# Kernel tuning notes

Hardware: AMD Instinct MI355X
Metric: run time of the kernel (lower is better)

## Reference

```python
import jax, jax.numpy as jnp
import numpy as np
from jax import lax

H = 1024      # hidden_size
M = 256       # memory_size
NH = 4        # num_heads
HD = M // NH  # head_dim = 64
EPS = 1e-5


def _ln(x, g, b):
    mu = jnp.mean(x, axis=-1, keepdims=True)
    var = jnp.mean(jnp.square(x - mu), axis=-1, keepdims=True)
    return (x - mu) * lax.rsqrt(var + EPS) * g + b


def setup_inputs() -> dict:
    key = jax.random.key(0)
    ks = jax.random.split(key, 12)
    B, S, NM = 8, 2048, 4096
    s = 0.02
    return {
        "query_hidden": jax.random.normal(ks[0], (B, S, H), jnp.float32),
        "mem_keys": jax.random.normal(ks[1], (NM, M), jnp.float32),
        "selection_scores": jax.random.uniform(ks[2], (NM,), jnp.float32),
        "qp_w": jax.random.normal(ks[3], (M, H), jnp.float32) * s,
        "qp_b": jnp.zeros((M,), jnp.float32),
        "in_proj_w": jax.random.normal(ks[4], (3 * M, M), jnp.float32) * s,
        "in_proj_b": jnp.zeros((3 * M,), jnp.float32),
        "out_w": jax.random.normal(ks[5], (M, M), jnp.float32) * s,
        "out_b": jnp.zeros((M,), jnp.float32),
        "gate_w": jax.random.normal(ks[6], (H, H + M), jnp.float32) * s,
        "gate_b": jnp.zeros((H,), jnp.float32),
        "int_w1": jax.random.normal(ks[7], (2 * H, H + M), jnp.float32) * s,
        "int_b1": jnp.zeros((2 * H,), jnp.float32),
        "int_ln_g": jnp.ones((2 * H,), jnp.float32),
        "int_ln_b": jnp.zeros((2 * H,), jnp.float32),
        "int_w2": jax.random.normal(ks[8], (H, 2 * H), jnp.float32) * s,
        "int_b2": jnp.zeros((H,), jnp.float32),
        "ln1_g": jnp.ones((M,), jnp.float32),
        "ln1_b": jnp.zeros((M,), jnp.float32),
        "ln2_g": jnp.ones((H,), jnp.float32),
        "ln2_b": jnp.zeros((H,), jnp.float32),
        "top_k": 512,
    }


def reference(query_hidden, mem_keys, selection_scores, qp_w, qp_b,
              in_proj_w, in_proj_b, out_w, out_b, gate_w, gate_b,
              int_w1, int_b1, int_ln_g, int_ln_b, int_w2, int_b2,
              ln1_g, ln1_b, ln2_g, ln2_b, top_k):
    B, S, _ = query_hidden.shape
    # query projection into memory space: [B,S,M]
    q_emb = query_hidden @ qp_w.T + qp_b
    # top-k memory selection by scores (static k)
    _, idx = lax.top_k(selection_scores, top_k)
    mem = mem_keys[idx]                      # [K, M]
    mem = _ln(mem, ln1_g, ln1_b)
    # MultiheadAttention (batch_first, eval mode). Per-position loop in the
    # original is equivalent to one batched attention (no mask).
    wq, wk, wv = jnp.split(in_proj_w, 3, axis=0)
    bq, bk, bv = jnp.split(in_proj_b, 3, axis=0)
    q = (q_emb @ wq.T + bq).reshape(B, S, NH, HD)
    k = (mem @ wk.T + bk).reshape(-1, NH, HD)   # [K,NH,HD]
    v = (mem @ wv.T + bv).reshape(-1, NH, HD)
    scores = jnp.einsum('bshd,khd->bhsk', q, k) / np.sqrt(HD).astype(jnp.float32)
    attn = jax.nn.softmax(scores, axis=-1)
    ctx = jnp.einsum('bhsk,khd->bshd', attn, v).reshape(B, S, M)
    attn_out = ctx @ out_w.T + out_b            # [B,S,M]
    # gated integration
    cat = jnp.concatenate([query_hidden, attn_out], axis=-1)  # [B,S,H+M]
    gate = jax.nn.sigmoid(cat @ gate_w.T + gate_b)
    h = _ln(cat @ int_w1.T + int_b1, int_ln_g, int_ln_b)
    h = jax.nn.gelu(h, approximate=False)
    integrated = h @ int_w2.T + int_b2
    out = _ln(query_hidden + gate * integrated, ln2_g, ln2_b)
    return out
```

## Files before the change

kernel.cpp:

```cpp
#include <hip/hip_runtime.h>
#include <math.h>


typedef __bf16 bf16x8 __attribute__((ext_vector_type(8)));
typedef __bf16 bf16x4 __attribute__((ext_vector_type(4)));
typedef float  floatx4 __attribute__((ext_vector_type(4)));

#define NMEM   4096
#define KSEL   512

__device__ __forceinline__ void gl_lds16(const __bf16* g, __bf16* l) {
  __builtin_amdgcn_global_load_lds(
      (const __attribute__((address_space(1))) void*)g,
      (__attribute__((address_space(3))) void*)l, 16, 0, 0);
}

__global__ void cvt_kernel(const float* __restrict__ s0, const float* __restrict__ s1,
                           const float* __restrict__ s2, const float* __restrict__ s3,
                           const float* __restrict__ s4,
                           __bf16* __restrict__ d0, __bf16* __restrict__ d1,
                           __bf16* __restrict__ d2, __bf16* __restrict__ d3,
                           __bf16* __restrict__ d4) {
  long q = (long)blockIdx.x * 256 + threadIdx.x;
  const long n0 = 16777216 / 4, n1 = 65536 / 4, n2 = 1310720 / 4,
             n3 = 2621440 / 4, n4 = 2097152 / 4;
  const float* s; __bf16* d; long off;
  if (q < n0) { s = s0; d = d0; off = q; }
  else if ((q -= n0) < n1) { s = s1; d = d1; off = q; }
  else if ((q -= n1) < n2) { s = s2; d = d2; off = q; }
  else if ((q -= n2) < n3) { s = s3; d = d3; off = q; }
  else if ((q -= n3) < n4) { s = s4; d = d4; off = q; }
  else return;
  float4 v = ((const float4*)s)[off];
  bf16x4 o;
  o[0] = (__bf16)v.x; o[1] = (__bf16)v.y; o[2] = (__bf16)v.z; o[3] = (__bf16)v.w;
  ((bf16x4*)d)[off] = o;
}

__device__ __forceinline__ unsigned mapbits(float x) {
  unsigned b = __float_as_uint(x);
  return (b & 0x80000000u) ? ~b : (b | 0x80000000u);
}

__global__ void topk_kernel(const float* __restrict__ scores, int* __restrict__ idx_out) {
  const int n = NMEM, k = KSEL;
  __shared__ int hist[256];
  __shared__ int s_need;
  __shared__ unsigned s_prefix;
  __shared__ int s_cnt_gt, s_ntie;
  __shared__ int tie[1024];
  int tid = threadIdx.x;
  if (tid == 0) { s_need = k; s_prefix = 0; s_cnt_gt = 0; s_ntie = 0; }
  __syncthreads();
  for (int pass = 0; pass < 4; ++pass) {
    if (tid < 256) hist[tid] = 0;
    __syncthreads();
    int shift = 24 - 8 * pass;
    unsigned pref = s_prefix;
    for (int i = tid; i < n; i += 256) {
      unsigned u = mapbits(scores[i]);
      bool in = (pass == 0) || ((u >> (shift + 8)) == pref);
      if (in) atomicAdd(&hist[(u >> shift) & 255], 1);
    }
    __syncthreads();
    if (tid == 0) {
      int need = s_need, above = 0, b = 255;
      for (;; --b) {
        int c = hist[b];
        if (above + c >= need) { s_need = need - above; break; }
        above += c;
      }
      s_prefix = (s_prefix << 8) | (unsigned)b;
    }
    __syncthreads();
  }
  unsigned T = s_prefix;
  int need = s_need;
  for (int i = tid; i < n; i += 256) {
    unsigned u = mapbits(scores[i]);
    if (u > T) { int p = atomicAdd(&s_cnt_gt, 1); idx_out[p] = i; }
    else if (u == T) { int t = atomicAdd(&s_ntie, 1); if (t < 1024) tie[t] = i; }
  }
  __syncthreads();
  int base = s_cnt_gt;
  int nt = s_ntie < 1024 ? s_ntie : 1024;
  for (int j = tid; j < nt; j += 256) {
    int my = tie[j], rank = 0;
    for (int l = 0; l < nt; ++l) rank += (tie[l] < my) ? 1 : 0;
    if (rank < need) idx_out[base + rank] = my;
  }
}

__global__ void wc_build(const float* __restrict__ qp_w, const float* __restrict__ qp_b,
                         const float* __restrict__ in_w, const float* __restrict__ in_b,
                         __bf16* __restrict__ Wc, float* __restrict__ bcq) {
  int i = blockIdx.x, t = threadIdx.x;
  const float* wq = in_w + (long)i * 256;
  float a0 = 0, a1 = 0, a2 = 0, a3 = 0;
  for (int s = 0; s < 256; ++s) {
    float wv = wq[s];
    const float* qr = qp_w + (long)s * 1024 + t;
    a0 += wv * qr[0];   a1 += wv * qr[256];
    a2 += wv * qr[512]; a3 += wv * qr[768];
  }
  __bf16* wr = Wc + (long)i * 1024 + t;
  wr[0]   = (__bf16)(0.125f * a0); wr[256] = (__bf16)(0.125f * a1);
  wr[512] = (__bf16)(0.125f * a2); wr[768] = (__bf16)(0.125f * a3);
  if (t == 0) {
    float s = in_b[i];
    for (int j = 0; j < 256; ++j) s += wq[j] * qp_b[j];
    bcq[i] = 0.125f * s;
  }
}

__global__ void kv_build(const int* __restrict__ idx, const float* __restrict__ mem_keys,
                         const float* __restrict__ in_w, const float* __restrict__ in_b,
                         const float* __restrict__ ln1g, const float* __restrict__ ln1b,
                         __bf16* __restrict__ Kmat, __bf16* __restrict__ Vt) {
  int r = blockIdx.x, t = threadIdx.x;
  int lane = t & 63, wave = t >> 6;
  __shared__ float wred[8];
  __shared__ float m[256];
  int row = idx[r];
  float x = mem_keys[(long)row * 256 + t];
  float s = x;
  #pragma unroll
  for (int o = 32; o > 0; o >>= 1) s += __shfl_xor(s, o);
  if (lane == 0) wred[wave] = s;
  __syncthreads();
  float mu = (wred[0] + wred[1] + wred[2] + wred[3]) / 256.0f;
  float e = x - mu;
  s = e * e;
  #pragma unroll
  for (int o = 32; o > 0; o >>= 1) s += __shfl_xor(s, o);
  if (lane == 0) wred[4 + wave] = s;
  __syncthreads();
  float rstd = rsqrtf((wred[4] + wred[5] + wred[6] + wred[7]) / 256.0f + 1e-5f);
  m[t] = e * rstd * ln1g[t] + ln1b[t];
  __syncthreads();
  float ka = 0.f, va = 0.f;
  const float* wk = in_w + (long)(256 + t) * 256;
  const float* wv = in_w + (long)(512 + t) * 256;
  #pragma unroll 4
  for (int i = 0; i < 256; i += 4) {
    float4 wkv = *(const float4*)(wk + i);
    float4 wvv = *(const float4*)(wv + i);
    ka += m[i] * wkv.x + m[i + 1] * wkv.y + m[i + 2] * wkv.z + m[i + 3] * wkv.w;
    va += m[i] * wvv.x + m[i + 1] * wvv.y + m[i + 2] * wvv.z + m[i + 3] * wvv.w;
  }
  ka += in_b[256 + t]; va += in_b[512 + t];
  Kmat[(long)r * 256 + t] = (__bf16)ka;
  Vt[(long)(t >> 6) * (64 * 512) + (long)(t & 63) * 512 + r] = (__bf16)va;
}

template <int BM, int BN, int EPI>
__launch_bounds__(256, 4)
__global__ void gemm_kernel(const __bf16* __restrict__ X1, int ldx1, int K1,
                            const __bf16* __restrict__ X2, int ldx2,
                            const __bf16* __restrict__ W, int ldw,
                            const float* __restrict__ bias,
                            __bf16* __restrict__ C, int ldc, int Ktot,
                            long sXz, long sWz, long sCz) {
  constexpr int BK = 64;
  __shared__ __bf16 As[BM * BK];
  __shared__ __bf16 Bs[BN * BK];
  const int tid = threadIdx.x;
  const int lane = tid & 63, wave = tid >> 6;
  const int wm = wave >> 1, wn = wave & 1;
  constexpr int FM = (BM / 2) / 16, FN = (BN / 2) / 16;
  floatx4 acc[FM][FN];
  #pragma unroll
  for (int i = 0; i < FM; ++i)
    #pragma unroll
    for (int j = 0; j < FN; ++j)
      #pragma unroll
      for (int r = 0; r < 4; ++r) acc[i][j][r] = 0.0f;

  const long z = blockIdx.z;
  const __bf16* x1 = X1 + z * sXz;
  const __bf16* w  = W + z * sWz;
  __bf16* c = C + z * sCz;
  const long row0 = (long)blockIdx.x * BM;
  const int col0 = blockIdx.y * BN;
  const int nKt = Ktot / BK;
  const int srow = lane >> 3;
  const int scol = ((lane & 7) ^ srow) * 8;

  for (int kt = 0; kt < nKt; ++kt) {
    const int k0 = kt * BK;
    const __bf16* xb; long xld; int kx;
    if (k0 < K1) { xb = x1; xld = ldx1; kx = k0; }
    else         { xb = X2; xld = ldx2; kx = k0 - K1; }
    #pragma unroll
    for (int i = 0; i < BM / 32; ++i) {
      int chunk = wave * (BM / 32) + i;
      const __bf16* g = xb + (row0 + chunk * 8 + srow) * xld + kx + scol;
      gl_lds16(g, As + chunk * 512);
    }
    #pragma unroll
    for (int i = 0; i < BN / 32; ++i) {
      int chunk = wave * (BN / 32) + i;
      const __bf16* g = w + (long)(col0 + chunk * 8 + srow) * ldw + k0 + scol;
      gl_lds16(g, Bs + chunk * 512);
    }
    __syncthreads();
    #pragma unroll
    for (int kk = 0; kk < 2; ++kk) {
      bf16x8 a[FM], b[FN];
      const int ccq = kk * 4 + (lane >> 4);
      #pragma unroll
      for (int fm = 0; fm < FM; ++fm) {
        const int r = wm * (BM / 2) + fm * 16 + (lane & 15);
        a[fm] = *(const bf16x8*)(As + r * BK + ((ccq ^ (r & 7)) << 3));
      }
      #pragma unroll
      for (int fn = 0; fn < FN; ++fn) {
        const int r = wn * (BN / 2) + fn * 16 + (lane & 15);
        b[fn] = *(const bf16x8*)(Bs + r * BK + ((ccq ^ (r & 7)) << 3));
      }
      #pragma unroll
      for (int fm = 0; fm < FM; ++fm)
        #pragma unroll
        for (int fn = 0; fn < FN; ++fn)
          acc[fm][fn] = __builtin_amdgcn_mfma_f32_16x16x32_bf16(a[fm], b[fn], acc[fm][fn], 0, 0, 0);
    }
    __syncthreads();
  }
  #pragma unroll
  for (int fn = 0; fn < FN; ++fn) {
    const int col = col0 + wn * (BN / 2) + fn * 16 + (lane & 15);
    float bv = (EPI == 1) ? 0.0f : bias[col];
    #pragma unroll
    for (int fm = 0; fm < FM; ++fm) {
      #pragma unroll
      for (int r = 0; r < 4; ++r) {
        long row = row0 + wm * (BM / 2) + fm * 16 + (lane >> 4) * 4 + r;
        float v = acc[fm][fn][r] + bv;
        if (EPI == 2) v = 1.0f / (1.0f + __expf(-v));
        c[row * (long)ldc + col] = (__bf16)v;
      }
    }
  }
}

__global__ void softmax_kernel(__bf16* __restrict__ S) {
  long row = (long)blockIdx.x * 4 + (threadIdx.x >> 6);
  int lane = threadIdx.x & 63;
  __bf16* p = S + row * 512 + lane * 8;
  bf16x8 v = *(const bf16x8*)p;
  float f[8], mx = -1e30f;
  #pragma unroll
  for (int j = 0; j < 8; ++j) { f[j] = (float)v[j]; mx = fmaxf(mx, f[j]); }
  #pragma unroll
  for (int o = 32; o > 0; o >>= 1) mx = fmaxf(mx, __shfl_xor(mx, o));
  float s = 0.f;
  #pragma unroll
  for (int j = 0; j < 8; ++j) { f[j] = __expf(f[j] - mx); s += f[j]; }
  #pragma unroll
  for (int o = 32; o > 0; o >>= 1) s += __shfl_xor(s, o);
  float inv = 1.0f / s;
  bf16x8 o8;
  #pragma unroll
  for (int j = 0; j < 8; ++j) o8[j] = (__bf16)(f[j] * inv);
  *(bf16x8*)p = o8;
}

__global__ void ln_gelu_kernel(__bf16* __restrict__ T1, const float* __restrict__ g,
                               const float* __restrict__ b) {
  long row = blockIdx.x; int t = threadIdx.x;
  int lane = t & 63, wave = t >> 6;
  __shared__ float wred[8];
  __bf16* p = T1 + row * 2048 + t * 8;
  bf16x8 v = *(const bf16x8*)p;
  float f[8], s = 0.f;
  #pragma unroll
  for (int j = 0; j < 8; ++j) { f[j] = (float)v[j]; s += f[j]; }
  #pragma unroll
  for (int o = 32; o > 0; o >>= 1) s += __shfl_xor(s, o);
  if (lane == 0) wred[wave] = s;
  __syncthreads();
  float mu = (wred[0] + wred[1] + wred[2] + wred[3]) / 2048.0f;
  s = 0.f;
  #pragma unroll
  for (int j = 0; j < 8; ++j) { f[j] -= mu; s += f[j] * f[j]; }
  #pragma unroll
  for (int o = 32; o > 0; o >>= 1) s += __shfl_xor(s, o);
  if (lane == 0) wred[4 + wave] = s;
  __syncthreads();
  float rstd = rsqrtf((wred[4] + wred[5] + wred[6] + wred[7]) / 2048.0f + 1e-5f);
  float4 g0 = *(const float4*)(g + t * 8), g1 = *(const float4*)(g + t * 8 + 4);
  float4 b0 = *(const float4*)(b + t * 8), b1 = *(const float4*)(b + t * 8 + 4);
  float gg[8] = { g0.x, g0.y, g0.z, g0.w, g1.x, g1.y, g1.z, g1.w };
  float bb[8] = { b0.x, b0.y, b0.z, b0.w, b1.x, b1.y, b1.z, b1.w };
  bf16x8 o8;
  #pragma unroll
  for (int j = 0; j < 8; ++j) {
    float y = f[j] * rstd * gg[j] + bb[j];
    float u = 1.5957691216057308f * (y + 0.044715f * y * y * y);
    o8[j] = (__bf16)(y / (1.0f + __expf(-u)));
  }
  *(bf16x8*)p = o8;
}

__global__ void final_kernel(const float* __restrict__ qh, const __bf16* __restrict__ gate,
                             const __bf16* __restrict__ integ, const float* __restrict__ g,
                             const float* __restrict__ b, float* __restrict__ out) {
  long row = blockIdx.x; int t = threadIdx.x;
  int lane = t & 63, wave = t >> 6;
  __shared__ float wred[8];
  long base = row * 1024 + t * 4;
  float4 q = *(const float4*)(qh + base);
  bf16x4 gv = *(const bf16x4*)(gate + base);
  bf16x4 iv = *(const bf16x4*)(integ + base);
  float f[4] = { q.x + (float)gv[0] * (float)iv[0], q.y + (float)gv[1] * (float)iv[1],
                 q.z + (float)gv[2] * (float)iv[2], q.w + (float)gv[3] * (float)iv[3] };
  float s = f[0] + f[1] + f[2] + f[3];
  #pragma unroll
  for (int o = 32; o > 0; o >>= 1) s += __shfl_xor(s, o);
  if (lane == 0) wred[wave] = s;
  __syncthreads();
  float mu = (wred[0] + wred[1] + wred[2] + wred[3]) / 1024.0f;
  s = 0.f;
  #pragma unroll
  for (int j = 0; j < 4; ++j) { f[j] -= mu; s += f[j] * f[j]; }
  #pragma unroll
  for (int o = 32; o > 0; o >>= 1) s += __shfl_xor(s, o);
  if (lane == 0) wred[4 + wave] = s;
  __syncthreads();
  float rstd = rsqrtf((wred[4] + wred[5] + wred[6] + wred[7]) / 1024.0f + 1e-5f);
  float4 gv4 = *(const float4*)(g + t * 4);
  float4 bv4 = *(const float4*)(b + t * 4);
  float4 ov;
  ov.x = f[0] * rstd * gv4.x + bv4.x;
  ov.y = f[1] * rstd * gv4.y + bv4.y;
  ov.z = f[2] * rstd * gv4.z + bv4.z;
  ov.w = f[3] * rstd * gv4.w + bv4.w;
  *(float4*)(out + base) = ov;
}

extern "C" void kernel_launch(void* const* d_in, const int* in_sizes, int n_in,
                              void* d_out, int out_size, void* d_ws, size_t ws_size,
                              hipStream_t stream) {
  const float* qh   = (const float*)d_in[0];
  const float* memk = (const float*)d_in[1];
  const float* sel  = (const float*)d_in[2];
  const float* qp_w = (const float*)d_in[3];
  const float* qp_b = (const float*)d_in[4];
  const float* inw  = (const float*)d_in[5];
  const float* inb  = (const float*)d_in[6];
  const float* outw = (const float*)d_in[7];
  const float* outb = (const float*)d_in[8];
  const float* gw   = (const float*)d_in[9];
  const float* gb   = (const float*)d_in[10];
  const float* w1   = (const float*)d_in[11];
  const float* b1   = (const float*)d_in[12];
  const float* lng  = (const float*)d_in[13];
  const float* lnb  = (const float*)d_in[14];
  const float* w2   = (const float*)d_in[15];
  const float* b2   = (const float*)d_in[16];
  const float* ln1g = (const float*)d_in[17];
  const float* ln1b = (const float*)d_in[18];
  const float* ln2g = (const float*)d_in[19];
  const float* ln2b = (const float*)d_in[20];
  float* out = (float*)d_out;
  char* ws = (char*)d_ws;

  const size_t IDX_O   = 0;
  const size_t BCQ_O   = 2048;
  const size_t WCB_O   = 3072;
  const size_t KMAT_O  = 527360;
  const size_t VT_O    = 789504;
  const size_t OUTWB_O = 1051648;
  const size_t GATEW_O = 1182720;
  const size_t INTW1_O = 3804160;
  const size_t INTW2_O = 9047040;
  const size_t QHB_O   = 13241344;
  const size_t QB_O    = 46795776;
  const size_t SB_O    = 55184384;
  const size_t CTX_O   = 122293248;
  const size_t ATTN_O  = 130681856;
  const size_t GATE_O  = 139070464;

  int*    idxb   = (int*)(ws + IDX_O);
  float*  bcq    = (float*)(ws + BCQ_O);
  __bf16* wcb    = (__bf16*)(ws + WCB_O);
  __bf16* kmat   = (__bf16*)(ws + KMAT_O);
  __bf16* vt     = (__bf16*)(ws + VT_O);
  __bf16* outwb  = (__bf16*)(ws + OUTWB_O);
  __bf16* gatewb = (__bf16*)(ws + GATEW_O);
  __bf16* intw1b = (__bf16*)(ws + INTW1_O);
  __bf16* intw2b = (__bf16*)(ws + INTW2_O);
  __bf16* qhb    = (__bf16*)(ws + QHB_O);
  __bf16* integb = (__bf16*)(ws + QHB_O);
  __bf16* qb     = (__bf16*)(ws + QB_O);
  __bf16* sb     = (__bf16*)(ws + SB_O);
  __bf16* t1b    = (__bf16*)(ws + SB_O);
  __bf16* ctxb   = (__bf16*)(ws + CTX_O);
  __bf16* attnb  = (__bf16*)(ws + ATTN_O);
  __bf16* gateb  = (__bf16*)(ws + GATE_O);

  cvt_kernel<<<22336, 256, 0, stream>>>(qh, outw, gw, w1, w2,
                                        qhb, outwb, gatewb, intw1b, intw2b);
  topk_kernel<<<1, 256, 0, stream>>>(sel, idxb);
  wc_build<<<256, 256, 0, stream>>>(qp_w, qp_b, inw, inb, wcb, bcq);
  kv_build<<<512, 256, 0, stream>>>(idxb, memk, inw, inb, ln1g, ln1b, kmat, vt);
  gemm_kernel<128, 128, 0><<<dim3(128, 2, 1), 256, 0, stream>>>(
      qhb, 1024, 1024, (const __bf16*)nullptr, 0, wcb, 1024, bcq, qb, 256, 1024, 0, 0, 0);
  gemm_kernel<128, 128, 1><<<dim3(128, 4, 4), 256, 0, stream>>>(
      qb, 256, 64, (const __bf16*)nullptr, 0, kmat, 256, (const float*)nullptr,
      sb, 512, 64, 64, 64, (long)16384 * 512);
  softmax_kernel<<<16384, 256, 0, stream>>>(sb);
  gemm_kernel<128, 64, 1><<<dim3(128, 1, 4), 256, 0, stream>>>(
      sb, 512, 512, (const __bf16*)nullptr, 0, vt, 512, (const float*)nullptr,
      ctxb, 256, 512, (long)16384 * 512, (long)64 * 512, 64);
  gemm_kernel<128, 128, 0><<<dim3(128, 2, 1), 256, 0, stream>>>(
      ctxb, 256, 256, (const __bf16*)nullptr, 0, outwb, 256, outb, attnb, 256, 256, 0, 0, 0);
  gemm_kernel<128, 128, 2><<<dim3(128, 8, 1), 256, 0, stream>>>(
      qhb, 1024, 1024, attnb, 256, gatewb, 1280, gb, gateb, 1024, 1280, 0, 0, 0);
  gemm_kernel<128, 128, 0><<<dim3(128, 16, 1), 256, 0, stream>>>(
      qhb, 1024, 1024, attnb, 256, intw1b, 1280, b1, t1b, 2048, 1280, 0, 0, 0);
  ln_gelu_kernel<<<16384, 256, 0, stream>>>(t1b, lng, lnb);
  gemm_kernel<128, 128, 0><<<dim3(128, 8, 1), 256, 0, stream>>>(
      t1b, 2048, 2048, (const __bf16*)nullptr, 0, intw2b, 2048, b2, integb, 1024, 2048, 0, 0, 0);
  final_kernel<<<16384, 256, 0, stream>>>(qh, gateb, integb, ln2g, ln2b, out);
}
```

Before: 633.7 us.

## Fuse attention into flash kernel and gate multiply into final GEMM epilogue

Replaces the separate QK^T GEMM, softmax, and PV GEMM with a single flash-attention kernel that keeps scores in LDS and uses an online softmax, so the 16384x512x4 score matrix is never written to or read from HBM. The gate multiply moves into the int_w2 GEMM epilogue, which lets the final LayerNorm kernel read one bf16 tensor instead of two. The small Q-projection and out-projection GEMMs switch to 64-row tiles to launch more blocks. In exchange, the flash kernel syncs several times per key chunk and uses a modest tile size.

```diff
diff --git a/kernel.cpp b/kernel.cpp
--- a/kernel.cpp
+++ b/kernel.cpp
@@ -159,6 +159,7 @@
                             const __bf16* __restrict__ X2, int ldx2,
                             const __bf16* __restrict__ W, int ldw,
                             const float* __restrict__ bias,
+                            const __bf16* __restrict__ gmul,
                             __bf16* __restrict__ C, int ldc, int Ktot,
                             long sXz, long sWz, long sCz) {
   constexpr int BK = 64;
@@ -237,32 +238,185 @@
         long row = row0 + wm * (BM / 2) + fm * 16 + (lane >> 4) * 4 + r;
         float v = acc[fm][fn][r] + bv;
         if (EPI == 2) v = 1.0f / (1.0f + __expf(-v));
+        if (EPI == 3) v *= (float)gmul[row * (long)ldc + col];
         c[row * (long)ldc + col] = (__bf16)v;
       }
     }
   }
 }
 
-__global__ void softmax_kernel(__bf16* __restrict__ S) {
-  long row = (long)blockIdx.x * 4 + (threadIdx.x >> 6);
-  int lane = threadIdx.x & 63;
-  __bf16* p = S + row * 512 + lane * 8;
-  bf16x8 v = *(const bf16x8*)p;
-  float f[8], mx = -1e30f;
-  #pragma unroll
-  for (int j = 0; j < 8; ++j) { f[j] = (float)v[j]; mx = fmaxf(mx, f[j]); }
-  #pragma unroll
-  for (int o = 32; o > 0; o >>= 1) mx = fmaxf(mx, __shfl_xor(mx, o));
-  float s = 0.f;
-  #pragma unroll
-  for (int j = 0; j < 8; ++j) { f[j] = __expf(f[j] - mx); s += f[j]; }
-  #pragma unroll
-  for (int o = 32; o > 0; o >>= 1) s += __shfl_xor(s, o);
-  float inv = 1.0f / s;
-  bf16x8 o8;
-  #pragma unroll
-  for (int j = 0; j < 8; ++j) o8[j] = (__bf16)(f[j] * inv);
-  *(bf16x8*)p = o8;
+__launch_bounds__(256, 2)
+__global__ void flash_kernel(const __bf16* __restrict__ Q, const __bf16* __restrict__ Km,
+                             const __bf16* __restrict__ Vt, __bf16* __restrict__ Ctx) {
+  __shared__ __bf16 Qs[64 * 64];
+  __shared__ __bf16 Ks[128 * 64];
+  __shared__ __bf16 Vs[64 * 128];
+  __shared__ __bf16 Ps[64 * 128];
+  __shared__ float mpart[2][64], spart[2][64];
+  __shared__ float m_run[64], l_run[64];
+  const int tid = threadIdx.x, lane = tid & 63, wave = tid >> 6;
+  const int wm = wave >> 1, wn = wave & 1;
+  const long row0 = (long)blockIdx.x * 64;
+  const int h = blockIdx.y;
+  const int srow = lane >> 3, scc = lane & 7;
+  const int q4 = lane >> 4, l15 = lane & 15;
+
+  if (tid < 64) { m_run[tid] = -3e38f; l_run[tid] = 0.f; }
+  #pragma unroll
+  for (int i = 0; i < 2; ++i) {
+    int chunk = wave * 2 + i;
+    int r = chunk * 8 + srow;
+    gl_lds16(Q + (row0 + r) * 256 + h * 64 + ((scc ^ (r & 7)) << 3), Qs + chunk * 512);
+  }
+  floatx4 oacc[2][2];
+  #pragma unroll
+  for (int fm = 0; fm < 2; ++fm)
+    #pragma unroll
+    for (int fn = 0; fn < 2; ++fn)
+      #pragma unroll
+      for (int r = 0; r < 4; ++r) oacc[fm][fn][r] = 0.f;
+
+  for (int c = 0; c < 4; ++c) {
+    #pragma unroll
+    for (int i = 0; i < 4; ++i) {
+      int chunk = wave * 4 + i;
+      int r = chunk * 8 + srow;
+      gl_lds16(Km + (long)(c * 128 + r) * 256 + h * 64 + ((scc ^ (r & 7)) << 3),
+               Ks + chunk * 512);
+    }
+    #pragma unroll
+    for (int i = 0; i < 4; ++i) {
+      int chunk = wave * 4 + i;
+      int d = chunk * 4 + q4;
+      int cc = l15 ^ (d & 7);
+      gl_lds16(Vt + (long)h * 32768 + (long)d * 512 + c * 128 + cc * 8,
+               Vs + chunk * 512);
+    }
+    __syncthreads();
+
+    floatx4 sacc[2][4];
+    #pragma unroll
+    for (int fm = 0; fm < 2; ++fm)
+      #pragma unroll
+      for (int fn = 0; fn < 4; ++fn)
+        #pragma unroll
+        for (int r = 0; r < 4; ++r) sacc[fm][fn][r] = 0.f;
+    #pragma unroll
+    for (int kk = 0; kk < 2; ++kk) {
+      bf16x8 a[2], b[4];
+      const int ccq = kk * 4 + q4;
+      #pragma unroll
+      for (int fm = 0; fm < 2; ++fm) {
+        const int r = wm * 32 + fm * 16 + l15;
+        a[fm] = *(const bf16x8*)(Qs + r * 64 + ((ccq ^ (r & 7)) << 3));
+      }
+      #pragma unroll
+      for (int fn = 0; fn < 4; ++fn) {
+        const int r = wn * 64 + fn * 16 + l15;
+        b[fn] = *(const bf16x8*)(Ks + r * 64 + ((ccq ^ (r & 7)) << 3));
+      }
+      #pragma unroll
+      for (int fm = 0; fm < 2; ++fm)
+        #pragma unroll
+        for (int fn = 0; fn < 4; ++fn)
+          sacc[fm][fn] = __builtin_amdgcn_mfma_f32_16x16x32_bf16(a[fm], b[fn], sacc[fm][fn], 0, 0, 0);
+    }
+    #pragma unroll
+    for (int fm = 0; fm < 2; ++fm) {
+      #pragma unroll
+      for (int r = 0; r < 4; ++r) {
+        float v = sacc[fm][0][r];
+        #pragma unroll
+        for (int fn = 1; fn < 4; ++fn) v = fmaxf(v, sacc[fm][fn][r]);
+        v = fmaxf(v, __shfl_xor(v, 1)); v = fmaxf(v, __shfl_xor(v, 2));
+        v = fmaxf(v, __shfl_xor(v, 4)); v = fmaxf(v, __shfl_xor(v, 8));
+        if (l15 == 0) mpart[wn][wm * 32 + fm * 16 + q4 * 4 + r] = v;
+      }
+    }
+    __syncthreads();
+
+    float nm[2][4], al[2][4], rs[2][4];
+    #pragma unroll
+    for (int fm = 0; fm < 2; ++fm)
+      #pragma unroll
+      for (int r = 0; r < 4; ++r) {
+        int row = wm * 32 + fm * 16 + q4 * 4 + r;
+        float pm = fmaxf(mpart[0][row], mpart[1][row]);
+        float mo = m_run[row];
+        float x = fmaxf(mo, pm);
+        nm[fm][r] = x;
+        al[fm][r] = __expf(mo - x);
+        rs[fm][r] = 0.f;
+      }
+    #pragma unroll
+    for (int fm = 0; fm < 2; ++fm)
+      #pragma unroll
+      for (int fn = 0; fn < 4; ++fn)
+        #pragma unroll
+        for (int r = 0; r < 4; ++r) {
+          float p = __expf(sacc[fm][fn][r] - nm[fm][r]);
+          rs[fm][r] += p;
+          int row = wm * 32 + fm * 16 + q4 * 4 + r;
+          int key = wn * 64 + fn * 16 + l15;
+          Ps[row * 128 + (((key >> 3) ^ (row & 7)) << 3) + (key & 7)] = (__bf16)p;
+        }
+    #pragma unroll
+    for (int fm = 0; fm < 2; ++fm)
+      #pragma unroll
+      for (int r = 0; r < 4; ++r) {
+        float v = rs[fm][r];
+        v += __shfl_xor(v, 1); v += __shfl_xor(v, 2);
+        v += __shfl_xor(v, 4); v += __shfl_xor(v, 8);
+        if (l15 == 0) spart[wn][wm * 32 + fm * 16 + q4 * 4 + r] = v;
+      }
+    __syncthreads();
+
+    #pragma unroll
+    for (int fm = 0; fm < 2; ++fm)
+      #pragma unroll
+      for (int r = 0; r < 4; ++r) {
+        int row = wm * 32 + fm * 16 + q4 * 4 + r;
+        if (wn == 0 && l15 == 0) {
+          m_run[row] = nm[fm][r];
+          l_run[row] = l_run[row] * al[fm][r] + spart[0][row] + spart[1][row];
+        }
+        #pragma unroll
+        for (int fn = 0; fn < 2; ++fn) oacc[fm][fn][r] *= al[fm][r];
+      }
+    #pragma unroll
+    for (int step = 0; step < 4; ++step) {
+      bf16x8 a[2], b[2];
+      const int ccq = step * 4 + q4;
+      #pragma unroll
+      for (int fm = 0; fm < 2; ++fm) {
+        const int r = wm * 32 + fm * 16 + l15;
+        a[fm] = *(const bf16x8*)(Ps + r * 128 + ((ccq ^ (r & 7)) << 3));
+      }
+      #pragma unroll
+      for (int fn = 0; fn < 2; ++fn) {
+        const int rv = wn * 32 + fn * 16 + l15;
+        b[fn] = *(const bf16x8*)(Vs + rv * 128 + ((ccq ^ (rv & 7)) << 3));
+      }
+      #pragma unroll
+      for (int fm = 0; fm < 2; ++fm)
+        #pragma unroll
+        for (int fn = 0; fn < 2; ++fn)
+          oacc[fm][fn] = __builtin_amdgcn_mfma_f32_16x16x32_bf16(a[fm], b[fn], oacc[fm][fn], 0, 0, 0);
+    }
+    __syncthreads();
+  }
+  #pragma unroll
+  for (int fm = 0; fm < 2; ++fm)
+    #pragma unroll
+    for (int r = 0; r < 4; ++r) {
+      int row = wm * 32 + fm * 16 + q4 * 4 + r;
+      float inv = 1.0f / l_run[row];
+      #pragma unroll
+      for (int fn = 0; fn < 2; ++fn) {
+        int col = wn * 32 + fn * 16 + l15;
+        Ctx[(row0 + row) * 256 + h * 64 + col] = (__bf16)(oacc[fm][fn][r] * inv);
+      }
+    }
 }
 
 __global__ void ln_gelu_kernel(__bf16* __restrict__ T1, const float* __restrict__ g,
@@ -302,18 +456,17 @@
   *(bf16x8*)p = o8;
 }
 
-__global__ void final_kernel(const float* __restrict__ qh, const __bf16* __restrict__ gate,
-                             const __bf16* __restrict__ integ, const float* __restrict__ g,
-                             const float* __restrict__ b, float* __restrict__ out) {
+__global__ void final_kernel(const float* __restrict__ qh, const __bf16* __restrict__ gi,
+                             const float* __restrict__ g, const float* __restrict__ b,
+                             float* __restrict__ out) {
   long row = blockIdx.x; int t = threadIdx.x;
   int lane = t & 63, wave = t >> 6;
   __shared__ float wred[8];
   long base = row * 1024 + t * 4;
   float4 q = *(const float4*)(qh + base);
-  bf16x4 gv = *(const bf16x4*)(gate + base);
-  bf16x4 iv = *(const bf16x4*)(integ + base);
-  float f[4] = { q.x + (float)gv[0] * (float)iv[0], q.y + (float)gv[1] * (float)iv[1],
-                 q.z + (float)gv[2] * (float)iv[2], q.w + (float)gv[3] * (float)iv[3] };
+  bf16x4 gv = *(const bf16x4*)(gi + base);
+  float f[4] = { q.x + (float)gv[0], q.y + (float)gv[1],
+                 q.z + (float)gv[2], q.w + (float)gv[3] };
   float s = f[0] + f[1] + f[2] + f[3];
   #pragma unroll
   for (int o = 32; o > 0; o >>= 1) s += __shfl_xor(s, o);
@@ -391,36 +544,30 @@
   __bf16* intw1b = (__bf16*)(ws + INTW1_O);
   __bf16* intw2b = (__bf16*)(ws + INTW2_O);
   __bf16* qhb    = (__bf16*)(ws + QHB_O);
-  __bf16* integb = (__bf16*)(ws + QHB_O);
+  __bf16* gib    = (__bf16*)(ws + QHB_O);
   __bf16* qb     = (__bf16*)(ws + QB_O);
-  __bf16* sb     = (__bf16*)(ws + SB_O);
   __bf16* t1b    = (__bf16*)(ws + SB_O);
   __bf16* ctxb   = (__bf16*)(ws + CTX_O);
   __bf16* attnb  = (__bf16*)(ws + ATTN_O);
   __bf16* gateb  = (__bf16*)(ws + GATE_O);
+  const __bf16* nullb = nullptr;
 
   cvt_kernel<<<22336, 256, 0, stream>>>(qh, outw, gw, w1, w2,
                                         qhb, outwb, gatewb, intw1b, intw2b);
   topk_kernel<<<1, 256, 0, stream>>>(sel, idxb);
   wc_build<<<256, 256, 0, stream>>>(qp_w, qp_b, inw, inb, wcb, bcq);
   kv_build<<<512, 256, 0, stream>>>(idxb, memk, inw, inb, ln1g, ln1b, kmat, vt);
-  gemm_kernel<128, 128, 0><<<dim3(128, 2, 1), 256, 0, stream>>>(
-      qhb, 1024, 1024, (const __bf16*)nullptr, 0, wcb, 1024, bcq, qb, 256, 1024, 0, 0, 0);
-  gemm_kernel<128, 128, 1><<<dim3(128, 4, 4), 256, 0, stream>>>(
-      qb, 256, 64, (const __bf16*)nullptr, 0, kmat, 256, (const float*)nullptr,
-      sb, 512, 64, 64, 64, (long)16384 * 512);
-  softmax_kernel<<<16384, 256, 0, stream>>>(sb);
-  gemm_kernel<128, 64, 1><<<dim3(128, 1, 4), 256, 0, stream>>>(
-      sb, 512, 512, (const __bf16*)nullptr, 0, vt, 512, (const float*)nullptr,
-      ctxb, 256, 512, (long)16384 * 512, (long)64 * 512, 64);
-  gemm_kernel<128, 128, 0><<<dim3(128, 2, 1), 256, 0, stream>>>(
-      ctxb, 256, 256, (const __bf16*)nullptr, 0, outwb, 256, outb, attnb, 256, 256, 0, 0, 0);
+  gemm_kernel<64, 128, 0><<<dim3(256, 2, 1), 256, 0, stream>>>(
+      qhb, 1024, 1024, nullb, 0, wcb, 1024, bcq, nullb, qb, 256, 1024, 0, 0, 0);
+  flash_kernel<<<dim3(256, 4, 1), 256, 0, stream>>>(qb, kmat, vt, ctxb);
+  gemm_kernel<64, 128, 0><<<dim3(256, 2, 1), 256, 0, stream>>>(
+      ctxb, 256, 256, nullb, 0, outwb, 256, outb, nullb, attnb, 256, 256, 0, 0, 0);
   gemm_kernel<128, 128, 2><<<dim3(128, 8, 1), 256, 0, stream>>>(
-      qhb, 1024, 1024, attnb, 256, gatewb, 1280, gb, gateb, 1024, 1280, 0, 0, 0);
+      qhb, 1024, 1024, attnb, 256, gatewb, 1280, gb, nullb, gateb, 1024, 1280, 0, 0, 0);
   gemm_kernel<128, 128, 0><<<dim3(128, 16, 1), 256, 0, stream>>>(
-      qhb, 1024, 1024, attnb, 256, intw1b, 1280, b1, t1b, 2048, 1280, 0, 0, 0);
+      qhb, 1024, 1024, attnb, 256, intw1b, 1280, b1, nullb, t1b, 2048, 1280, 0, 0, 0);
   ln_gelu_kernel<<<16384, 256, 0, stream>>>(t1b, lng, lnb);
-  gemm_kernel<128, 128, 0><<<dim3(128, 8, 1), 256, 0, stream>>>(
-      t1b, 2048, 2048, (const __bf16*)nullptr, 0, intw2b, 2048, b2, integb, 1024, 2048, 0, 0, 0);
-  final_kernel<<<16384, 256, 0, stream>>>(qh, gateb, integb, ln2g, ln2b, out);
-}
+  gemm_kernel<128, 128, 3><<<dim3(128, 8, 1), 256, 0, stream>>>(
+      t1b, 2048, 2048, nullb, 0, intw2b, 2048, b2, gateb, gib, 1024, 2048, 0, 0, 0);
+  final_kernel<<<16384, 256, 0, stream>>>(qh, gib, ln2g, ln2b, out);
+}
```

Result: no change. 643.6 us (+1.6%).
